# Kernel tuning notes

Measured on AMD Instinct MI355X. Metric: run time of the kernel, lower is better.

## Reference

```python
import jax, jax.numpy as jnp
import numpy as np

S = 2048
NODE_DIM = 128
H = 8          # num_heads
C = 32         # num_channels


def setup_inputs() -> dict:
    key = jax.random.key(0)
    ks = jax.random.split(key, 12)
    inv = lambda n: 1.0 / np.sqrt(n)
    inp = {
        "nodes": jax.random.normal(ks[0], (S, NODE_DIM), dtype=jnp.float32),
        "pos": jax.random.uniform(ks[1], (S, 3), dtype=jnp.float32),
        "rot": jax.random.normal(ks[2], (S, 4), dtype=jnp.float32),
        # eqx.nn.Linear weights are (out_features, in_features)
        "w_nodes_kq": jax.random.uniform(ks[3], (H * C * 2, NODE_DIM), minval=-inv(NODE_DIM), maxval=inv(NODE_DIM)),
        "b_nodes_kq": jax.random.uniform(ks[4], (H * C * 2,), minval=-inv(NODE_DIM), maxval=inv(NODE_DIM)),
        "w_pos_kq": jax.random.uniform(ks[5], (H * C * 2, 6), minval=-inv(6), maxval=inv(6)),
        "b_pos_kq": jax.random.uniform(ks[6], (H * C * 2,), minval=-inv(6), maxval=inv(6)),
        "w_rot_kq": jax.random.uniform(ks[7], (H * C * 2, 4), minval=-inv(4), maxval=inv(4)),  # no bias
        "w_values": jax.random.uniform(ks[8], (NODE_DIM * H * 3, NODE_DIM), minval=-inv(NODE_DIM), maxval=inv(NODE_DIM)),
        "b_values": jax.random.uniform(ks[9], (NODE_DIM * H * 3,), minval=-inv(NODE_DIM), maxval=inv(NODE_DIM)),
    }
    return inp


def reference(nodes, pos, rot, w_nodes_kq, b_nodes_kq, w_pos_kq, b_pos_kq,
              w_rot_kq, w_values, b_values):
    seq_len = nodes.shape[0]
    # circular positional features: [S, 6]
    pos_feat = jnp.concatenate([jnp.cos(2 * jnp.pi * pos), jnp.sin(2 * jnp.pi * pos)], axis=-1)

    # values: [S, 3H, node_dim]
    val = (nodes @ w_values.T + b_values).reshape(seq_len, 3 * H, -1)

    # per-source k/q projections, each -> [S, H, C]
    nodes_k, nodes_q = jnp.split((nodes @ w_nodes_kq.T + b_nodes_kq).reshape(seq_len, H, -1), 2, -1)
    pos_k, pos_q = jnp.split((pos_feat @ w_pos_kq.T + b_pos_kq).reshape(seq_len, H, -1), 2, -1)
    rot_k, rot_q = jnp.split((rot @ w_rot_kq.T).reshape(seq_len, H, -1), 2, -1)

    # concat over head axis -> [S, 3H, C]
    k = jnp.concatenate([nodes_k, pos_k, rot_k], axis=-2)
    q = jnp.concatenate([nodes_q, pos_q, rot_q], axis=-2)

    # logits: [S, S, 3H]; square the last H (rotation) heads' sub-logits
    logits = jnp.einsum('ihc,jhc->ijh', k, q)
    logits = logits.at[..., -H:].set(jnp.square(logits[..., -H:]))

    # softmax over j (axis=-2), then weighted sum of values over j and heads
    att = jax.nn.softmax(logits, axis=-2)
    out = jnp.einsum('ijh,jhd->id', att, val)  # [S, node_dim]
    return out
```

## Files before the change

kernel.cpp:

```cpp
#include <hip/hip_runtime.h>
#include <hip/hip_bf16.h>
#include <math.h>

#define SEQ 2048
#define NHEAD 24
#define CDIM 32
#define VDIM 128

typedef short bf16x8 __attribute__((ext_vector_type(8)));
typedef float f32x4 __attribute__((ext_vector_type(4)));

#define L2E 1.44269504088896f
#define SQRT_L2E 1.20112240878645f

#if __has_builtin(__builtin_amdgcn_exp2f)
#define EXP2(x) __builtin_amdgcn_exp2f(x)
#else
#define EXP2(x) exp2f(x)
#endif

__device__ unsigned short g_kkp[(size_t)24 * 128 * 2 * 64 * 8];
__device__ unsigned short g_qv[(size_t)24 * 32 * 24 * 64 * 8];
__device__ unsigned short g_wp[(size_t)224 * 4 * 2 * 64 * 8];
__device__ unsigned short g_np[(size_t)128 * 4 * 2 * 64 * 8];

__device__ __forceinline__ unsigned short f2b(float x) {
  union { float f; unsigned u; } v; v.f = x;
  unsigned r = v.u + 0x7FFF + ((v.u >> 16) & 1);
  return (unsigned short)(r >> 16);
}
__device__ __forceinline__ float b2f(unsigned short u) {
  union { unsigned u32; float f; } x; x.u32 = ((unsigned)u) << 16; return x.f;
}
__device__ __forceinline__ unsigned pk2(float a, float b) {
  __hip_bfloat162 t = __float22bfloat162_rn(float2{a, b});
  union { __hip_bfloat162 h; unsigned u; } c; c.h = t; return c.u;
}
__device__ __forceinline__ unsigned long long pack64(const float* p) {
  return ((unsigned long long)pk2(p[2], p[3]) << 32) | pk2(p[0], p[1]);
}
__device__ __forceinline__ float bperm_f(int srclane, float v) {
  union { float f; int i; } u; u.f = v;
  u.i = __builtin_amdgcn_ds_bpermute(srclane * 4, u.i);
  return u.f;
}
__device__ __forceinline__ void gld16(const unsigned short* g, unsigned short* l) {
  __builtin_amdgcn_global_load_lds(
      (const __attribute__((address_space(1))) unsigned int*)g,
      (__attribute__((address_space(3))) unsigned int*)l, 16, 0, 0);
}

__global__ __launch_bounds__(256) void k_prep(const float* __restrict__ nodes,
                                              const float* __restrict__ w_v,
                                              const float* __restrict__ w_n) {
  const int tid = blockIdx.x * 256 + threadIdx.x;
  const int fg = tid >> 6, lane = tid & 63;
  const int e0 = (lane >> 4) * 8;
  const float* p;
  unsigned short* dst;
  if (blockIdx.x < 224) {
    const int colblk = fg >> 2, ks = fg & 3;
    const int ocol = colblk * 16 + (lane & 15);
    const float* src = (ocol < 3072) ? (w_v + (size_t)ocol * 128)
                                     : (w_n + (size_t)(ocol - 3072) * 128);
    p = src + ks * 32 + e0;
    dst = g_wp + (size_t)fg * 1024;
  } else {
    const int fg2 = fg - 224 * 4;
    const int rowblk = fg2 >> 2, ks = fg2 & 3;
    p = nodes + (size_t)(rowblk * 16 + (lane & 15)) * 128 + ks * 32 + e0;
    dst = g_np + (size_t)fg2 * 1024;
  }
  float4 f0 = *(const float4*)p;
  float4 f1 = *(const float4*)(p + 4);
  float ff[8] = {f0.x, f0.y, f0.z, f0.w, f1.x, f1.y, f1.z, f1.w};
  bf16x8 hi, lo;
#pragma unroll
  for (int e = 0; e < 8; ++e) {
    unsigned short h2 = f2b(ff[e]);
    hi[e] = (short)h2;
    lo[e] = (short)f2b(ff[e] - b2f(h2));
  }
  *(bf16x8*)(dst + (size_t)lane * 8) = hi;
  *(bf16x8*)(dst + 512 + (size_t)lane * 8) = lo;
}

__global__ __launch_bounds__(256) void k_proj(const float* __restrict__ b_v,
                                              const float* __restrict__ b_n) {
  const int jt = blockIdx.x;
  const int bo = blockIdx.y;
  const bool is_kq = bo >= 48;
  const float* bsrc = is_kq ? b_n : b_v;
  const int o0b = is_kq ? (bo - 48) * 64 : bo * 64;
  const int tx = threadIdx.x;
  const int w = tx >> 6, lane = tx & 63;
  const int m = lane & 15, quad = lane >> 4;

  __shared__ __align__(16) unsigned short bst[32][64][8];
  __shared__ __align__(16) float res[4][64][20];

  const unsigned short* wp = g_wp + ((size_t)bo * 32 + w * 8) * 512 + (size_t)lane * 8;
#pragma unroll
  for (int s = 0; s < 8; ++s)
    gld16(wp + s * 512, &bst[w * 8 + s][0][0]);

  bf16x8 ah[4], al[4];
  const unsigned short* np = g_np + (size_t)(jt * 4 + w) * 4096 + (size_t)lane * 8;
#pragma unroll
  for (int ks = 0; ks < 4; ++ks) {
    ah[ks] = *(const bf16x8*)(np + ks * 1024);
    al[ks] = *(const bf16x8*)(np + ks * 1024 + 512);
  }
  __syncthreads();

  f32x4 C[4];
#pragma unroll
  for (int ob = 0; ob < 4; ++ob) {
    f32x4 acc = {0.f, 0.f, 0.f, 0.f};
#pragma unroll
    for (int ks = 0; ks < 4; ++ks) {
      bf16x8 bh = *(const bf16x8*)&bst[ob * 8 + ks * 2][lane][0];
      bf16x8 bl = *(const bf16x8*)&bst[ob * 8 + ks * 2 + 1][lane][0];
      acc = __builtin_amdgcn_mfma_f32_16x16x32_bf16(ah[ks], bh, acc, 0, 0, 0);
      acc = __builtin_amdgcn_mfma_f32_16x16x32_bf16(al[ks], bh, acc, 0, 0, 0);
      acc = __builtin_amdgcn_mfma_f32_16x16x32_bf16(ah[ks], bl, acc, 0, 0, 0);
    }
    C[ob] = acc;
  }
#pragma unroll
  for (int ob = 0; ob < 4; ++ob) {
    float bias = bsrc[o0b + ob * 16 + m];
#pragma unroll
    for (int r = 0; r < 4; ++r)
      res[w][ob * 16 + m][quad * 4 + r] = C[ob][r] + bias;
  }
  if (!is_kq) {
    const int g = bo >> 1, dbb = (bo & 1) * 4;
    const int jc = w >> 1, khb = (w & 1) * 2;
    const int rowq = quad;
#pragma unroll
    for (int oct = 0; oct < 2; ++oct) {
      f32x4 v0 = *(const f32x4*)&res[w][rowq * 16 + m][oct * 8];
      f32x4 v1 = *(const f32x4*)&res[w][rowq * 16 + m][oct * 8 + 4];
      bf16x8 pk;
#pragma unroll
      for (int e = 0; e < 4; ++e) {
        pk[e]     = (short)f2b(v0[e]);
        pk[4 + e] = (short)f2b(v1[e]);
      }
      ((bf16x8*)g_qv)[(((size_t)g * 32 + jt) * 24 + 8 + jc * 8 + dbb + rowq) * 64
                      + (khb + oct) * 16 + m] = pk;
    }
  } else {
    const int h = bo - 48;
    const int rowq = quad;
    {
      bf16x8 hi, lo;
#pragma unroll
      for (int e = 0; e < 8; ++e) {
        float v = res[w][rowq * 8 + e][m] * L2E;
        unsigned short h2 = f2b(v);
        hi[e] = (short)h2;
        lo[e] = (short)f2b(v - b2f(h2));
      }
      size_t base = ((size_t)(h * 128 + jt * 4 + w) * 2) * 512 + (size_t)(rowq * 16 + m) * 8;
      *(bf16x8*)(g_kkp + base) = hi;
      *(bf16x8*)(g_kkp + base + 512) = lo;
    }
    {
      bf16x8 hi, lo;
#pragma unroll
      for (int e = 0; e < 8; ++e) {
        float v = res[w][32 + rowq * 8 + e][m];
        unsigned short h2 = f2b(v);
        hi[e] = (short)h2;
        lo[e] = (short)f2b(v - b2f(h2));
      }
      size_t base = (((size_t)h * 32 + jt) * 24 + w * 2) * 512 + (size_t)(rowq * 16 + m) * 8;
      *(bf16x8*)(g_qv + base) = hi;
      *(bf16x8*)(g_qv + base + 512) = lo;
    }
  }
}

__device__ __forceinline__ void repack_store(const unsigned* __restrict__ res,
                                             int oh, int it16, int tx, int head_base) {
#pragma unroll
  for (int t2 = 0; t2 < 2; ++t2) {
    int cid = tx + t2 * 256;
    int hl  = cid >> 7;
    int kq  = (cid >> 6) & 1;
    int row = cid & 63;
    int m = row & 15, kb = row >> 4;
    int ob = hl * 64 + kq * 32 + kb * 8;
    bf16x8 hi, lo;
#pragma unroll
    for (int e = 0; e < 8; ++e) {
      unsigned pk = res[(ob + e) * 17 + m];
      hi[e] = (short)(pk >> 16);
      lo[e] = (short)(pk & 0xffff);
    }
    int gh = head_base + oh * 4 + hl;
    if (kq == 0) {
      size_t base = ((size_t)(gh * 128 + it16) * 2) * 512 + (size_t)row * 8;
      *(bf16x8*)(g_kkp + base) = hi;
      *(bf16x8*)(g_kkp + base + 512) = lo;
    } else {
      int jt = it16 >> 2, jb = it16 & 3;
      size_t base = (((size_t)gh * 32 + jt) * 24 + jb * 2) * 512 + (size_t)row * 8;
      *(bf16x8*)(g_qv + base) = hi;
      *(bf16x8*)(g_qv + base + 512) = lo;
    }
  }
}

__global__ __launch_bounds__(256) void k_posrot(const float* __restrict__ pos,
                                                const float* __restrict__ rot,
                                                const float* __restrict__ w_p,
                                                const float* __restrict__ b_p,
                                                const float* __restrict__ w_r) {
  const int it16 = blockIdx.x;
  const int oh   = blockIdx.y;
  const int br   = blockIdx.z;
  const int tx = threadIdx.x;
  const int i0 = it16 * 16;

  __shared__ float pf_sh[16][8];
  __shared__ float rr_sh[16][4];
  __shared__ unsigned res[256 * 17];

  if (br == 0) {
    if (tx < 48) {
      int r = tx / 3, t = tx - r * 3;
      float p = pos[(i0 + r) * 3 + t];
      pf_sh[r][t]     = cosf(6.283185307179586f * p);
      pf_sh[r][t + 3] = sinf(6.283185307179586f * p);
    }
  } else {
    if (tx < 64) {
      int r = tx >> 2, t = tx & 3;
      rr_sh[r][t] = rot[(i0 + r) * 4 + t];
    }
  }
  __syncthreads();

  const int og = tx & 63, ig = tx >> 6;

  if (br == 0) {
#pragma unroll
    for (int oo = 0; oo < 4; ++oo) {
      int o = oh * 256 + oo * 64 + og;
      float bb = b_p[o];
      float w0 = w_p[o * 6 + 0], w1 = w_p[o * 6 + 1], w2 = w_p[o * 6 + 2];
      float w3 = w_p[o * 6 + 3], w4 = w_p[o * 6 + 4], w5 = w_p[o * 6 + 5];
      float sc = ((o & 63) < 32) ? L2E : 1.f;
#pragma unroll
      for (int ii = 0; ii < 4; ++ii) {
        int i = ig * 4 + ii;
        float v = bb + pf_sh[i][0] * w0 + pf_sh[i][1] * w1 + pf_sh[i][2] * w2
                     + pf_sh[i][3] * w3 + pf_sh[i][4] * w4 + pf_sh[i][5] * w5;
        v *= sc;
        unsigned short hi = f2b(v);
        unsigned short lo = f2b(v - b2f(hi));
        res[(oo * 64 + og) * 17 + i] = ((unsigned)hi << 16) | lo;
      }
    }
  } else {
#pragma unroll
    for (int oo = 0; oo < 4; ++oo) {
      int o = oh * 256 + oo * 64 + og;
      float w0 = w_r[o * 4 + 0], w1 = w_r[o * 4 + 1], w2 = w_r[o * 4 + 2], w3 = w_r[o * 4 + 3];
      float sc = ((o & 63) < 32) ? SQRT_L2E : 1.f;
#pragma unroll
      for (int ii = 0; ii < 4; ++ii) {
        int i = ig * 4 + ii;
        float v = (rr_sh[i][0] * w0 + rr_sh[i][1] * w1 + rr_sh[i][2] * w2 + rr_sh[i][3] * w3) * sc;
        unsigned short hi = f2b(v);
        unsigned short lo = f2b(v - b2f(hi));
        res[(oo * 64 + og) * 17 + i] = ((unsigned)hi << 16) | lo;
      }
    }
  }
  __syncthreads();
  repack_store(res, oh, it16, tx, 8 + br * 8);
}

__global__ __launch_bounds__(256) void k_zero(float* __restrict__ out) {
  out[blockIdx.x * 256 + threadIdx.x] = 0.f;
}

__global__ __launch_bounds__(256, 3) void k_attn(float* __restrict__ out) {
  const int it = blockIdx.x;
  const int g  = blockIdx.y;
  const int tx = threadIdx.x;
  const int w = tx >> 6, lane = tx & 63;
  const int quad = lane >> 4, n = lane & 15;
  const int iblk = it * 4 + w;

  __shared__ __align__(16) unsigned short stage[2][24][64][8];
  __shared__ __align__(16) unsigned long long p_lds[4][64][2];

  const bf16x8* kp = (const bf16x8*)g_kkp + (size_t)(g * 128 + iblk) * 2 * 64;
  const bf16x8 khi = kp[lane], klo = kp[64 + lane];

  f32x4 oacc[8];
#pragma unroll
  for (int db = 0; db < 8; ++db)
#pragma unroll
    for (int r = 0; r < 4; ++r) oacc[db][r] = 0.f;

  float m_run = -3.0e38f, l_part = 0.f;
  const bool is_rot = (g >= 16);
  const int pin = (lane & 56) | ((lane ^ (lane >> 3)) & 7);
  const int wrow0 = (quad >> 1) * 16 + n;
  const int wrow1 = wrow0 + 32;
  const int pr0 = (wrow0 & 56) | ((wrow0 ^ (wrow0 >> 3)) & 7);
  const int pr1 = (wrow1 & 56) | ((wrow1 ^ (wrow1 >> 3)) & 7);
  const int whalf = quad & 1;

  const unsigned short* qv = g_qv + ((size_t)g * 32 * 24 + w * 6) * 512 + (size_t)lane * 8;

#define STG(nb)                                          \
  { gld16(qv,             &stage[nb][w * 6 + 0][0][0]);  \
    gld16(qv + 512,       &stage[nb][w * 6 + 1][0][0]);  \
    gld16(qv + 1024,      &stage[nb][w * 6 + 2][0][0]);  \
    gld16(qv + 1536,      &stage[nb][w * 6 + 3][0][0]);  \
    gld16(qv + 2048,      &stage[nb][w * 6 + 4][0][0]);  \
    gld16(qv + 2560,      &stage[nb][w * 6 + 5][0][0]); }

  STG(0)

  bf16x8 a0 = {}, a1 = {};
  bf16x8 vprev[16];

  for (int jt = 0; jt < 32; ++jt) {
    const int buf = jt & 1;
    __syncthreads();

    if (jt) {
#pragma unroll
      for (int db = 0; db < 8; ++db)
        oacc[db] = __builtin_amdgcn_mfma_f32_16x16x32_bf16(a0, vprev[db], oacc[db], 0, 0, 0);
#pragma unroll
      for (int db = 0; db < 8; ++db)
        oacc[db] = __builtin_amdgcn_mfma_f32_16x16x32_bf16(a1, vprev[8 + db], oacc[db], 0, 0, 0);
    }

    qv += 24 * 512;
    if (jt < 31) STG(buf ^ 1)

    const bf16x8* st = (const bf16x8*)&stage[buf][0][0][0];
    f32x4 S[4];
#pragma unroll
    for (int jb = 0; jb < 4; ++jb) {
      bf16x8 qh = st[(jb * 2) * 64 + lane], ql = st[(jb * 2 + 1) * 64 + lane];
      f32x4 a = {0.f, 0.f, 0.f, 0.f};
      a = __builtin_amdgcn_mfma_f32_16x16x32_bf16(qh, khi, a, 0, 0, 0);
      a = __builtin_amdgcn_mfma_f32_16x16x32_bf16(ql, khi, a, 0, 0, 0);
      a = __builtin_amdgcn_mfma_f32_16x16x32_bf16(qh, klo, a, 0, 0, 0);
      S[jb] = a;
    }
    if (is_rot) {
#pragma unroll
      for (int jb = 0; jb < 4; ++jb)
#pragma unroll
        for (int r = 0; r < 4; ++r) S[jb][r] *= S[jb][r];
    }
    float mloc = S[0][0];
#pragma unroll
    for (int jb = 0; jb < 4; ++jb)
#pragma unroll
      for (int r = 0; r < 4; ++r) mloc = fmaxf(mloc, S[jb][r]);
    if (__ballot(mloc > m_run)) {
      float mb = fmaxf(mloc, __shfl_xor(mloc, 16));
      mb = fmaxf(mb, __shfl_xor(mb, 32));
      float m_new = fmaxf(m_run, mb);
      float alpha = EXP2(m_run - m_new);
      m_run = m_new;
      l_part *= alpha;
      f32x4 av;
#pragma unroll
      for (int r = 0; r < 4; ++r) av[r] = bperm_f(quad * 4 + r, alpha);
#pragma unroll
      for (int db = 0; db < 8; ++db) {
        oacc[db][0] *= av[0]; oacc[db][1] *= av[1];
        oacc[db][2] *= av[2]; oacc[db][3] *= av[3];
      }
    }
    float p[4][4];
#pragma unroll
    for (int jb = 0; jb < 4; ++jb)
#pragma unroll
      for (int r = 0; r < 4; ++r) {
        p[jb][r] = EXP2(S[jb][r] - m_run);
        l_part += p[jb][r];
      }
    p_lds[w][pr0][whalf] = pack64(p[0]);
    p_lds[w][pr1][whalf] = pack64(p[1]);
    a0 = *(const bf16x8*)&p_lds[w][pin][0];
    p_lds[w][pr0][whalf] = pack64(p[2]);
    p_lds[w][pr1][whalf] = pack64(p[3]);
    a1 = *(const bf16x8*)&p_lds[w][pin][0];
#pragma unroll
    for (int f = 0; f < 16; ++f) vprev[f] = st[(8 + f) * 64 + lane];
  }
#pragma unroll
  for (int db = 0; db < 8; ++db)
    oacc[db] = __builtin_amdgcn_mfma_f32_16x16x32_bf16(a0, vprev[db], oacc[db], 0, 0, 0);
#pragma unroll
  for (int db = 0; db < 8; ++db)
    oacc[db] = __builtin_amdgcn_mfma_f32_16x16x32_bf16(a1, vprev[8 + db], oacc[db], 0, 0, 0);

  float l = l_part;
  l += __shfl_xor(l, 16);
  l += __shfl_xor(l, 32);
  float linv = 1.f / l;
  f32x4 lv;
#pragma unroll
  for (int r = 0; r < 4; ++r) lv[r] = bperm_f(quad * 4 + r, linv);
  const int ibase = it * 64 + w * 16 + quad * 4;
#pragma unroll
  for (int db = 0; db < 8; ++db)
#pragma unroll
    for (int r = 0; r < 4; ++r)
      atomicAdd(&out[(size_t)(ibase + r) * VDIM + db * 16 + n], oacc[db][r] * lv[r]);
}

extern "C" void kernel_launch(void* const* d_in, const int* in_sizes, int n_in,
                              void* d_out, int out_size, void* d_ws, size_t ws_size,
                              hipStream_t stream) {
  const float* nodes = (const float*)d_in[0];
  const float* pos   = (const float*)d_in[1];
  const float* rot   = (const float*)d_in[2];
  const float* w_n   = (const float*)d_in[3];
  const float* b_n   = (const float*)d_in[4];
  const float* w_p   = (const float*)d_in[5];
  const float* b_p   = (const float*)d_in[6];
  const float* w_r   = (const float*)d_in[7];
  const float* w_v   = (const float*)d_in[8];
  const float* b_v   = (const float*)d_in[9];
  float* out = (float*)d_out;

  k_zero<<<dim3((SEQ * VDIM) / 256), 256, 0, stream>>>(out);
  k_prep<<<dim3(352), 256, 0, stream>>>(nodes, w_v, w_n);
  k_posrot<<<dim3(128, 2, 2), 256, 0, stream>>>(pos, rot, w_p, b_p, w_r);
  k_proj<<<dim3(32, 56), 256, 0, stream>>>(b_v, b_n);
  k_attn<<<dim3(32, NHEAD), 256, 0, stream>>>(out);
}
```

Before: 168.1 us.

## Fuse prep/projection launches and restructure attention to split keys across waves

The zero-fill kernel is merged into the prep kernel, and the pos/rot projection is merged with the node projection into one launch, so five launches become three. The attention kernel is reorganized so each wave covers all four query-row blocks for half of the key range and half of the value dimension. Q/V fragments are read directly from global memory with one-step prefetch instead of being staged through LDS with barriers. Partial softmax statistics from the two key halves are combined through shared memory at the end. This raises register pressure (launch bounds drop from 3 to 2 blocks per CU) and duplicates the exp/softmax work across the two value-dimension waves.

```diff
diff --git a/kernel.cpp b/kernel.cpp
--- a/kernel.cpp
+++ b/kernel.cpp
@@ -50,15 +50,19 @@
       (__attribute__((address_space(3))) unsigned int*)l, 16, 0, 0);
 }
 
-__global__ __launch_bounds__(256) void k_prep(const float* __restrict__ nodes,
-                                              const float* __restrict__ w_v,
-                                              const float* __restrict__ w_n) {
-  const int tid = blockIdx.x * 256 + threadIdx.x;
+__global__ __launch_bounds__(256) void k_pre(const float* __restrict__ nodes,
+                                             const float* __restrict__ w_v,
+                                             const float* __restrict__ w_n,
+                                             float* __restrict__ out) {
+  const int bx = blockIdx.x;
+  if (bx < 1024) { out[bx * 256 + threadIdx.x] = 0.f; return; }
+  const int bb = bx - 1024;
+  const int tid = bb * 256 + threadIdx.x;
   const int fg = tid >> 6, lane = tid & 63;
   const int e0 = (lane >> 4) * 8;
   const float* p;
   unsigned short* dst;
-  if (blockIdx.x < 224) {
+  if (bb < 224) {
     const int colblk = fg >> 2, ks = fg & 3;
     const int ocol = colblk * 16 + (lane & 15);
     const float* src = (ocol < 3072) ? (w_v + (size_t)ocol * 128)
@@ -85,104 +89,6 @@
   *(bf16x8*)(dst + 512 + (size_t)lane * 8) = lo;
 }
 
-__global__ __launch_bounds__(256) void k_proj(const float* __restrict__ b_v,
-                                              const float* __restrict__ b_n) {
-  const int jt = blockIdx.x;
-  const int bo = blockIdx.y;
-  const bool is_kq = bo >= 48;
-  const float* bsrc = is_kq ? b_n : b_v;
-  const int o0b = is_kq ? (bo - 48) * 64 : bo * 64;
-  const int tx = threadIdx.x;
-  const int w = tx >> 6, lane = tx & 63;
-  const int m = lane & 15, quad = lane >> 4;
-
-  __shared__ __align__(16) unsigned short bst[32][64][8];
-  __shared__ __align__(16) float res[4][64][20];
-
-  const unsigned short* wp = g_wp + ((size_t)bo * 32 + w * 8) * 512 + (size_t)lane * 8;
-#pragma unroll
-  for (int s = 0; s < 8; ++s)
-    gld16(wp + s * 512, &bst[w * 8 + s][0][0]);
-
-  bf16x8 ah[4], al[4];
-  const unsigned short* np = g_np + (size_t)(jt * 4 + w) * 4096 + (size_t)lane * 8;
-#pragma unroll
-  for (int ks = 0; ks < 4; ++ks) {
-    ah[ks] = *(const bf16x8*)(np + ks * 1024);
-    al[ks] = *(const bf16x8*)(np + ks * 1024 + 512);
-  }
-  __syncthreads();
-
-  f32x4 C[4];
-#pragma unroll
-  for (int ob = 0; ob < 4; ++ob) {
-    f32x4 acc = {0.f, 0.f, 0.f, 0.f};
-#pragma unroll
-    for (int ks = 0; ks < 4; ++ks) {
-      bf16x8 bh = *(const bf16x8*)&bst[ob * 8 + ks * 2][lane][0];
-      bf16x8 bl = *(const bf16x8*)&bst[ob * 8 + ks * 2 + 1][lane][0];
-      acc = __builtin_amdgcn_mfma_f32_16x16x32_bf16(ah[ks], bh, acc, 0, 0, 0);
-      acc = __builtin_amdgcn_mfma_f32_16x16x32_bf16(al[ks], bh, acc, 0, 0, 0);
-      acc = __builtin_amdgcn_mfma_f32_16x16x32_bf16(ah[ks], bl, acc, 0, 0, 0);
-    }
-    C[ob] = acc;
-  }
-#pragma unroll
-  for (int ob = 0; ob < 4; ++ob) {
-    float bias = bsrc[o0b + ob * 16 + m];
-#pragma unroll
-    for (int r = 0; r < 4; ++r)
-      res[w][ob * 16 + m][quad * 4 + r] = C[ob][r] + bias;
-  }
-  if (!is_kq) {
-    const int g = bo >> 1, dbb = (bo & 1) * 4;
-    const int jc = w >> 1, khb = (w & 1) * 2;
-    const int rowq = quad;
-#pragma unroll
-    for (int oct = 0; oct < 2; ++oct) {
-      f32x4 v0 = *(const f32x4*)&res[w][rowq * 16 + m][oct * 8];
-      f32x4 v1 = *(const f32x4*)&res[w][rowq * 16 + m][oct * 8 + 4];
-      bf16x8 pk;
-#pragma unroll
-      for (int e = 0; e < 4; ++e) {
-        pk[e]     = (short)f2b(v0[e]);
-        pk[4 + e] = (short)f2b(v1[e]);
-      }
-      ((bf16x8*)g_qv)[(((size_t)g * 32 + jt) * 24 + 8 + jc * 8 + dbb + rowq) * 64
-                      + (khb + oct) * 16 + m] = pk;
-    }
-  } else {
-    const int h = bo - 48;
-    const int rowq = quad;
-    {
-      bf16x8 hi, lo;
-#pragma unroll
-      for (int e = 0; e < 8; ++e) {
-        float v = res[w][rowq * 8 + e][m] * L2E;
-        unsigned short h2 = f2b(v);
-        hi[e] = (short)h2;
-        lo[e] = (short)f2b(v - b2f(h2));
-      }
-      size_t base = ((size_t)(h * 128 + jt * 4 + w) * 2) * 512 + (size_t)(rowq * 16 + m) * 8;
-      *(bf16x8*)(g_kkp + base) = hi;
-      *(bf16x8*)(g_kkp + base + 512) = lo;
-    }
-    {
-      bf16x8 hi, lo;
-#pragma unroll
-      for (int e = 0; e < 8; ++e) {
-        float v = res[w][32 + rowq * 8 + e][m];
-        unsigned short h2 = f2b(v);
-        hi[e] = (short)h2;
-        lo[e] = (short)f2b(v - b2f(h2));
-      }
-      size_t base = (((size_t)h * 32 + jt) * 24 + w * 2) * 512 + (size_t)(rowq * 16 + m) * 8;
-      *(bf16x8*)(g_qv + base) = hi;
-      *(bf16x8*)(g_qv + base + 512) = lo;
-    }
-  }
-}
-
 __device__ __forceinline__ void repack_store(const unsigned* __restrict__ res,
                                              int oh, int it16, int tx, int head_base) {
 #pragma unroll
@@ -191,8 +97,8 @@
     int hl  = cid >> 7;
     int kq  = (cid >> 6) & 1;
     int row = cid & 63;
-    int m = row & 15, kb = row >> 4;
-    int ob = hl * 64 + kq * 32 + kb * 8;
+    int m = row & 15;
+    int ob = hl * 64 + kq * 32 + (row >> 4) * 8;
     bf16x8 hi, lo;
 #pragma unroll
     for (int e = 0; e < 8; ++e) {
@@ -214,216 +120,324 @@
   }
 }
 
-__global__ __launch_bounds__(256) void k_posrot(const float* __restrict__ pos,
-                                                const float* __restrict__ rot,
-                                                const float* __restrict__ w_p,
-                                                const float* __restrict__ b_p,
-                                                const float* __restrict__ w_r) {
-  const int it16 = blockIdx.x;
-  const int oh   = blockIdx.y;
-  const int br   = blockIdx.z;
+__global__ __launch_bounds__(256) void k_mid(const float* __restrict__ b_v,
+                                             const float* __restrict__ b_n,
+                                             const float* __restrict__ pos,
+                                             const float* __restrict__ rot,
+                                             const float* __restrict__ w_p,
+                                             const float* __restrict__ b_p,
+                                             const float* __restrict__ w_r) {
+  __shared__ __align__(16) char smem[53248];
+  const int bx = blockIdx.x;
   const int tx = threadIdx.x;
-  const int i0 = it16 * 16;
-
-  __shared__ float pf_sh[16][8];
-  __shared__ float rr_sh[16][4];
-  __shared__ unsigned res[256 * 17];
-
-  if (br == 0) {
-    if (tx < 48) {
-      int r = tx / 3, t = tx - r * 3;
-      float p = pos[(i0 + r) * 3 + t];
-      pf_sh[r][t]     = cosf(6.283185307179586f * p);
-      pf_sh[r][t + 3] = sinf(6.283185307179586f * p);
+
+  if (bx < 1792) {
+    const int jt = bx & 31;
+    const int bo = bx >> 5;
+    const bool is_kq = bo >= 48;
+    const float* bsrc = is_kq ? b_n : b_v;
+    const int o0b = is_kq ? (bo - 48) * 64 : bo * 64;
+    const int w = tx >> 6, lane = tx & 63;
+    const int m = lane & 15, quad = lane >> 4;
+
+    unsigned short (*bst)[64][8] = (unsigned short(*)[64][8])smem;
+    float (*res)[64][20] = (float(*)[64][20])(smem + 32768);
+
+    const unsigned short* wp = g_wp + ((size_t)bo * 32 + w * 8) * 512 + (size_t)lane * 8;
+#pragma unroll
+    for (int s = 0; s < 8; ++s)
+      gld16(wp + s * 512, &bst[w * 8 + s][0][0]);
+
+    bf16x8 ah[4], al[4];
+    const unsigned short* np = g_np + (size_t)(jt * 4 + w) * 4096 + (size_t)lane * 8;
+#pragma unroll
+    for (int ks = 0; ks < 4; ++ks) {
+      ah[ks] = *(const bf16x8*)(np + ks * 1024);
+      al[ks] = *(const bf16x8*)(np + ks * 1024 + 512);
+    }
+    __syncthreads();
+
+    f32x4 C[4];
+#pragma unroll
+    for (int ob = 0; ob < 4; ++ob) {
+      f32x4 acc = {0.f, 0.f, 0.f, 0.f};
+#pragma unroll
+      for (int ks = 0; ks < 4; ++ks) {
+        bf16x8 bh = *(const bf16x8*)&bst[ob * 8 + ks * 2][lane][0];
+        bf16x8 bl = *(const bf16x8*)&bst[ob * 8 + ks * 2 + 1][lane][0];
+        acc = __builtin_amdgcn_mfma_f32_16x16x32_bf16(ah[ks], bh, acc, 0, 0, 0);
+        acc = __builtin_amdgcn_mfma_f32_16x16x32_bf16(al[ks], bh, acc, 0, 0, 0);
+        acc = __builtin_amdgcn_mfma_f32_16x16x32_bf16(ah[ks], bl, acc, 0, 0, 0);
+      }
+      C[ob] = acc;
+    }
+#pragma unroll
+    for (int ob = 0; ob < 4; ++ob) {
+      float bias = bsrc[o0b + ob * 16 + m];
+#pragma unroll
+      for (int r = 0; r < 4; ++r)
+        res[w][ob * 16 + m][quad * 4 + r] = C[ob][r] + bias;
+    }
+    if (!is_kq) {
+      const int g = bo >> 1, dbb = (bo & 1) * 4;
+      const int jc = w >> 1, khb = (w & 1) * 2;
+#pragma unroll
+      for (int oct = 0; oct < 2; ++oct) {
+        f32x4 v0 = *(const f32x4*)&res[w][quad * 16 + m][oct * 8];
+        f32x4 v1 = *(const f32x4*)&res[w][quad * 16 + m][oct * 8 + 4];
+        bf16x8 pk;
+#pragma unroll
+        for (int e = 0; e < 4; ++e) {
+          pk[e]     = (short)f2b(v0[e]);
+          pk[4 + e] = (short)f2b(v1[e]);
+        }
+        ((bf16x8*)g_qv)[(((size_t)g * 32 + jt) * 24 + 8 + jc * 8 + dbb + quad) * 64
+                        + (khb + oct) * 16 + m] = pk;
+      }
+    } else {
+      const int h = bo - 48;
+      {
+        bf16x8 hi, lo;
+#pragma unroll
+        for (int e = 0; e < 8; ++e) {
+          float v = res[w][quad * 8 + e][m] * L2E;
+          unsigned short h2 = f2b(v);
+          hi[e] = (short)h2;
+          lo[e] = (short)f2b(v - b2f(h2));
+        }
+        size_t base = ((size_t)(h * 128 + jt * 4 + w) * 2) * 512 + (size_t)(quad * 16 + m) * 8;
+        *(bf16x8*)(g_kkp + base) = hi;
+        *(bf16x8*)(g_kkp + base + 512) = lo;
+      }
+      {
+        bf16x8 hi, lo;
+#pragma unroll
+        for (int e = 0; e < 8; ++e) {
+          float v = res[w][32 + quad * 8 + e][m];
+          unsigned short h2 = f2b(v);
+          hi[e] = (short)h2;
+          lo[e] = (short)f2b(v - b2f(h2));
+        }
+        size_t base = (((size_t)h * 32 + jt) * 24 + w * 2) * 512 + (size_t)(quad * 16 + m) * 8;
+        *(bf16x8*)(g_qv + base) = hi;
+        *(bf16x8*)(g_qv + base + 512) = lo;
+      }
     }
   } else {
-    if (tx < 64) {
-      int r = tx >> 2, t = tx & 3;
-      rr_sh[r][t] = rot[(i0 + r) * 4 + t];
-    }
-  }
-  __syncthreads();
-
-  const int og = tx & 63, ig = tx >> 6;
-
-  if (br == 0) {
-#pragma unroll
-    for (int oo = 0; oo < 4; ++oo) {
-      int o = oh * 256 + oo * 64 + og;
-      float bb = b_p[o];
-      float w0 = w_p[o * 6 + 0], w1 = w_p[o * 6 + 1], w2 = w_p[o * 6 + 2];
-      float w3 = w_p[o * 6 + 3], w4 = w_p[o * 6 + 4], w5 = w_p[o * 6 + 5];
-      float sc = ((o & 63) < 32) ? L2E : 1.f;
-#pragma unroll
-      for (int ii = 0; ii < 4; ++ii) {
-        int i = ig * 4 + ii;
-        float v = bb + pf_sh[i][0] * w0 + pf_sh[i][1] * w1 + pf_sh[i][2] * w2
-                     + pf_sh[i][3] * w3 + pf_sh[i][4] * w4 + pf_sh[i][5] * w5;
-        v *= sc;
-        unsigned short hi = f2b(v);
-        unsigned short lo = f2b(v - b2f(hi));
-        res[(oo * 64 + og) * 17 + i] = ((unsigned)hi << 16) | lo;
-      }
-    }
-  } else {
-#pragma unroll
-    for (int oo = 0; oo < 4; ++oo) {
-      int o = oh * 256 + oo * 64 + og;
-      float w0 = w_r[o * 4 + 0], w1 = w_r[o * 4 + 1], w2 = w_r[o * 4 + 2], w3 = w_r[o * 4 + 3];
-      float sc = ((o & 63) < 32) ? SQRT_L2E : 1.f;
-#pragma unroll
-      for (int ii = 0; ii < 4; ++ii) {
-        int i = ig * 4 + ii;
-        float v = (rr_sh[i][0] * w0 + rr_sh[i][1] * w1 + rr_sh[i][2] * w2 + rr_sh[i][3] * w3) * sc;
-        unsigned short hi = f2b(v);
-        unsigned short lo = f2b(v - b2f(hi));
-        res[(oo * 64 + og) * 17 + i] = ((unsigned)hi << 16) | lo;
-      }
-    }
-  }
-  __syncthreads();
-  repack_store(res, oh, it16, tx, 8 + br * 8);
-}
-
-__global__ __launch_bounds__(256) void k_zero(float* __restrict__ out) {
-  out[blockIdx.x * 256 + threadIdx.x] = 0.f;
-}
-
-__global__ __launch_bounds__(256, 3) void k_attn(float* __restrict__ out) {
+    const int r0 = bx - 1792;
+    const int it16 = r0 & 127, oh = (r0 >> 7) & 1, br = r0 >> 8;
+    const int i0 = it16 * 16;
+    unsigned* res = (unsigned*)smem;
+    float (*pf_sh)[8] = (float(*)[8])(smem + 17408);
+    float (*rr_sh)[4] = (float(*)[4])(smem + 17920);
+
+    if (br == 0) {
+      if (tx < 48) {
+        int r = tx / 3, t = tx - r * 3;
+        float p = pos[(i0 + r) * 3 + t];
+        pf_sh[r][t]     = cosf(6.283185307179586f * p);
+        pf_sh[r][t + 3] = sinf(6.283185307179586f * p);
+      }
+    } else {
+      if (tx < 64) {
+        int r = tx >> 2, t = tx & 3;
+        rr_sh[r][t] = rot[(i0 + r) * 4 + t];
+      }
+    }
+    __syncthreads();
+
+    const int og = tx & 63, ig = tx >> 6;
+    if (br == 0) {
+#pragma unroll
+      for (int oo = 0; oo < 4; ++oo) {
+        int o = oh * 256 + oo * 64 + og;
+        float bb = b_p[o];
+        float w0 = w_p[o * 6 + 0], w1 = w_p[o * 6 + 1], w2 = w_p[o * 6 + 2];
+        float w3 = w_p[o * 6 + 3], w4 = w_p[o * 6 + 4], w5 = w_p[o * 6 + 5];
+        float sc = ((o & 63) < 32) ? L2E : 1.f;
+#pragma unroll
+        for (int ii = 0; ii < 4; ++ii) {
+          int i = ig * 4 + ii;
+          float v = bb + pf_sh[i][0] * w0 + pf_sh[i][1] * w1 + pf_sh[i][2] * w2
+                       + pf_sh[i][3] * w3 + pf_sh[i][4] * w4 + pf_sh[i][5] * w5;
+          v *= sc;
+          unsigned short hi = f2b(v);
+          unsigned short lo = f2b(v - b2f(hi));
+          res[(oo * 64 + og) * 17 + i] = ((unsigned)hi << 16) | lo;
+        }
+      }
+    } else {
+#pragma unroll
+      for (int oo = 0; oo < 4; ++oo) {
+        int o = oh * 256 + oo * 64 + og;
+        float w0 = w_r[o * 4 + 0], w1 = w_r[o * 4 + 1], w2 = w_r[o * 4 + 2], w3 = w_r[o * 4 + 3];
+        float sc = ((o & 63) < 32) ? SQRT_L2E : 1.f;
+#pragma unroll
+        for (int ii = 0; ii < 4; ++ii) {
+          int i = ig * 4 + ii;
+          float v = (rr_sh[i][0] * w0 + rr_sh[i][1] * w1 + rr_sh[i][2] * w2 + rr_sh[i][3] * w3) * sc;
+          unsigned short hi = f2b(v);
+          unsigned short lo = f2b(v - b2f(hi));
+          res[(oo * 64 + og) * 17 + i] = ((unsigned)hi << 16) | lo;
+        }
+      }
+    }
+    __syncthreads();
+    repack_store(res, oh, it16, tx, 8 + br * 8);
+  }
+}
+
+__global__ __launch_bounds__(256, 2) void k_attn(float* __restrict__ out) {
   const int it = blockIdx.x;
   const int g  = blockIdx.y;
   const int tx = threadIdx.x;
   const int w = tx >> 6, lane = tx & 63;
-  const int quad = lane >> 4, n = lane & 15;
-  const int iblk = it * 4 + w;
-
-  __shared__ __align__(16) unsigned short stage[2][24][64][8];
+  const int qd = lane >> 4, c = lane & 15;
+  const int jh = w >> 1, dh = w & 1;
+  const bool is_rot = (g >= 16);
+
   __shared__ __align__(16) unsigned long long p_lds[4][64][2];
-
-  const bf16x8* kp = (const bf16x8*)g_kkp + (size_t)(g * 128 + iblk) * 2 * 64;
-  const bf16x8 khi = kp[lane], klo = kp[64 + lane];
-
-  f32x4 oacc[8];
-#pragma unroll
-  for (int db = 0; db < 8; ++db)
-#pragma unroll
-    for (int r = 0; r < 4; ++r) oacc[db][r] = 0.f;
-
-  float m_run = -3.0e38f, l_part = 0.f;
-  const bool is_rot = (g >= 16);
+  __shared__ __align__(16) float s_m[2][4][16];
+  __shared__ __align__(16) float s_l[2][4][16];
+  __shared__ __align__(16) float s_sc[2][4][16];
+
+  bf16x8 khi[4], klo[4];
+#pragma unroll
+  for (int ib = 0; ib < 4; ++ib) {
+    const bf16x8* kp = (const bf16x8*)g_kkp + ((size_t)(g * 128 + it * 4 + ib)) * 2 * 64;
+    khi[ib] = kp[lane]; klo[ib] = kp[64 + lane];
+  }
+
+  f32x4 oacc[4][4];
+#pragma unroll
+  for (int ib = 0; ib < 4; ++ib)
+#pragma unroll
+    for (int d = 0; d < 4; ++d)
+#pragma unroll
+      for (int r = 0; r < 4; ++r) oacc[ib][d][r] = 0.f;
+
+  float m4[4] = {-3.0e38f, -3.0e38f, -3.0e38f, -3.0e38f};
+  float l4[4] = {0.f, 0.f, 0.f, 0.f};
+
   const int pin = (lane & 56) | ((lane ^ (lane >> 3)) & 7);
-  const int wrow0 = (quad >> 1) * 16 + n;
-  const int wrow1 = wrow0 + 32;
-  const int pr0 = (wrow0 & 56) | ((wrow0 ^ (wrow0 >> 3)) & 7);
-  const int pr1 = (wrow1 & 56) | ((wrow1 ^ (wrow1 >> 3)) & 7);
-  const int whalf = quad & 1;
-
-  const unsigned short* qv = g_qv + ((size_t)g * 32 * 24 + w * 6) * 512 + (size_t)lane * 8;
-
-#define STG(nb)                                          \
-  { gld16(qv,             &stage[nb][w * 6 + 0][0][0]);  \
-    gld16(qv + 512,       &stage[nb][w * 6 + 1][0][0]);  \
-    gld16(qv + 1024,      &stage[nb][w * 6 + 2][0][0]);  \
-    gld16(qv + 1536,      &stage[nb][w * 6 + 3][0][0]);  \
-    gld16(qv + 2048,      &stage[nb][w * 6 + 4][0][0]);  \
-    gld16(qv + 2560,      &stage[nb][w * 6 + 5][0][0]); }
-
-  STG(0)
-
-  bf16x8 a0 = {}, a1 = {};
-  bf16x8 vprev[16];
-
-  for (int jt = 0; jt < 32; ++jt) {
-    const int buf = jt & 1;
-    __syncthreads();
-
-    if (jt) {
-#pragma unroll
-      for (int db = 0; db < 8; ++db)
-        oacc[db] = __builtin_amdgcn_mfma_f32_16x16x32_bf16(a0, vprev[db], oacc[db], 0, 0, 0);
-#pragma unroll
-      for (int db = 0; db < 8; ++db)
-        oacc[db] = __builtin_amdgcn_mfma_f32_16x16x32_bf16(a1, vprev[8 + db], oacc[db], 0, 0, 0);
-    }
-
-    qv += 24 * 512;
-    if (jt < 31) STG(buf ^ 1)
-
-    const bf16x8* st = (const bf16x8*)&stage[buf][0][0][0];
-    f32x4 S[4];
-#pragma unroll
-    for (int jb = 0; jb < 4; ++jb) {
-      bf16x8 qh = st[(jb * 2) * 64 + lane], ql = st[(jb * 2 + 1) * 64 + lane];
+  const int row0 = (qd >> 1) * 16 + c;
+  const int row1 = row0 + 32;
+  const int pr0 = (row0 & 56) | ((row0 ^ (row0 >> 3)) & 7);
+  const int pr1 = (row1 & 56) | ((row1 ^ (row1 >> 3)) & 7);
+  const int half = qd & 1;
+
+  const unsigned short* gbase = g_qv + (size_t)g * 32 * 24 * 512 + (size_t)lane * 8;
+#define FRAG(jt_, slot_) (*(const bf16x8*)(gbase + ((size_t)(jt_) * 24 + (slot_)) * 512))
+
+  bf16x8 qf[4];
+#pragma unroll
+  for (int s = 0; s < 4; ++s) qf[s] = FRAG(jh * 16, s);
+
+  for (int t = 0; t < 32; ++t) {
+    const int jt = jh * 16 + (t >> 1), jc = t & 1;
+    bf16x8 vb[4];
+#pragma unroll
+    for (int d = 0; d < 4; ++d) vb[d] = FRAG(jt, 8 + jc * 8 + dh * 4 + d);
+    bf16x8 qn[4];
+    if (t < 31) {
+      const int jt1 = jh * 16 + ((t + 1) >> 1), jc1 = (t + 1) & 1;
+#pragma unroll
+      for (int s = 0; s < 4; ++s) qn[s] = FRAG(jt1, jc1 * 4 + s);
+    }
+    f32x4 S0[4], S1[4];
+#pragma unroll
+    for (int ib = 0; ib < 4; ++ib) {
       f32x4 a = {0.f, 0.f, 0.f, 0.f};
-      a = __builtin_amdgcn_mfma_f32_16x16x32_bf16(qh, khi, a, 0, 0, 0);
-      a = __builtin_amdgcn_mfma_f32_16x16x32_bf16(ql, khi, a, 0, 0, 0);
-      a = __builtin_amdgcn_mfma_f32_16x16x32_bf16(qh, klo, a, 0, 0, 0);
-      S[jb] = a;
+      a = __builtin_amdgcn_mfma_f32_16x16x32_bf16(qf[0], khi[ib], a, 0, 0, 0);
+      a = __builtin_amdgcn_mfma_f32_16x16x32_bf16(qf[1], khi[ib], a, 0, 0, 0);
+      a = __builtin_amdgcn_mfma_f32_16x16x32_bf16(qf[0], klo[ib], a, 0, 0, 0);
+      S0[ib] = a;
+      f32x4 b = {0.f, 0.f, 0.f, 0.f};
+      b = __builtin_amdgcn_mfma_f32_16x16x32_bf16(qf[2], khi[ib], b, 0, 0, 0);
+      b = __builtin_amdgcn_mfma_f32_16x16x32_bf16(qf[3], khi[ib], b, 0, 0, 0);
+      b = __builtin_amdgcn_mfma_f32_16x16x32_bf16(qf[2], klo[ib], b, 0, 0, 0);
+      S1[ib] = b;
     }
     if (is_rot) {
 #pragma unroll
-      for (int jb = 0; jb < 4; ++jb)
-#pragma unroll
-        for (int r = 0; r < 4; ++r) S[jb][r] *= S[jb][r];
-    }
-    float mloc = S[0][0];
-#pragma unroll
-    for (int jb = 0; jb < 4; ++jb)
-#pragma unroll
-      for (int r = 0; r < 4; ++r) mloc = fmaxf(mloc, S[jb][r]);
-    if (__ballot(mloc > m_run)) {
-      float mb = fmaxf(mloc, __shfl_xor(mloc, 16));
-      mb = fmaxf(mb, __shfl_xor(mb, 32));
-      float m_new = fmaxf(m_run, mb);
-      float alpha = EXP2(m_run - m_new);
-      m_run = m_new;
-      l_part *= alpha;
-      f32x4 av;
-#pragma unroll
-      for (int r = 0; r < 4; ++r) av[r] = bperm_f(quad * 4 + r, alpha);
-#pragma unroll
-      for (int db = 0; db < 8; ++db) {
-        oacc[db][0] *= av[0]; oacc[db][1] *= av[1];
-        oacc[db][2] *= av[2]; oacc[db][3] *= av[3];
-      }
-    }
-    float p[4][4];
-#pragma unroll
-    for (int jb = 0; jb < 4; ++jb)
+      for (int ib = 0; ib < 4; ++ib)
+#pragma unroll
+        for (int r = 0; r < 4; ++r) { S0[ib][r] *= S0[ib][r]; S1[ib][r] *= S1[ib][r]; }
+    }
+    float ml[4];
+#pragma unroll
+    for (int ib = 0; ib < 4; ++ib) {
+      float v = fmaxf(fmaxf(S0[ib][0], S0[ib][1]), fmaxf(S0[ib][2], S0[ib][3]));
+      v = fmaxf(v, fmaxf(fmaxf(S1[ib][0], S1[ib][1]), fmaxf(S1[ib][2], S1[ib][3])));
+      ml[ib] = v;
+    }
+    bool ex = (ml[0] > m4[0]) || (ml[1] > m4[1]) || (ml[2] > m4[2]) || (ml[3] > m4[3]);
+    if (__ballot(ex)) {
+#pragma unroll
+      for (int ib = 0; ib < 4; ++ib) {
+        float mb = fmaxf(ml[ib], __shfl_xor(ml[ib], 16));
+        mb = fmaxf(mb, __shfl_xor(mb, 32));
+        float mn = fmaxf(m4[ib], mb);
+        float al = EXP2(m4[ib] - mn);
+        m4[ib] = mn;
+        l4[ib] *= al;
+        f32x4 av;
+#pragma unroll
+        for (int r = 0; r < 4; ++r) av[r] = bperm_f(qd * 4 + r, al);
+#pragma unroll
+        for (int d = 0; d < 4; ++d) {
+          oacc[ib][d][0] *= av[0]; oacc[ib][d][1] *= av[1];
+          oacc[ib][d][2] *= av[2]; oacc[ib][d][3] *= av[3];
+        }
+      }
+    }
+#pragma unroll
+    for (int ib = 0; ib < 4; ++ib) {
+      f32x4 p0, p1;
 #pragma unroll
       for (int r = 0; r < 4; ++r) {
-        p[jb][r] = EXP2(S[jb][r] - m_run);
-        l_part += p[jb][r];
-      }
-    p_lds[w][pr0][whalf] = pack64(p[0]);
-    p_lds[w][pr1][whalf] = pack64(p[1]);
-    a0 = *(const bf16x8*)&p_lds[w][pin][0];
-    p_lds[w][pr0][whalf] = pack64(p[2]);
-    p_lds[w][pr1][whalf] = pack64(p[3]);
-    a1 = *(const bf16x8*)&p_lds[w][pin][0];
-#pragma unroll
-    for (int f = 0; f < 16; ++f) vprev[f] = st[(8 + f) * 64 + lane];
-  }
-#pragma unroll
-  for (int db = 0; db < 8; ++db)
-    oacc[db] = __builtin_amdgcn_mfma_f32_16x16x32_bf16(a0, vprev[db], oacc[db], 0, 0, 0);
-#pragma unroll
-  for (int db = 0; db < 8; ++db)
-    oacc[db] = __builtin_amdgcn_mfma_f32_16x16x32_bf16(a1, vprev[8 + db], oacc[db], 0, 0, 0);
-
-  float l = l_part;
-  l += __shfl_xor(l, 16);
-  l += __shfl_xor(l, 32);
-  float linv = 1.f / l;
-  f32x4 lv;
-#pragma unroll
-  for (int r = 0; r < 4; ++r) lv[r] = bperm_f(quad * 4 + r, linv);
-  const int ibase = it * 64 + w * 16 + quad * 4;
-#pragma unroll
-  for (int db = 0; db < 8; ++db)
-#pragma unroll
-    for (int r = 0; r < 4; ++r)
-      atomicAdd(&out[(size_t)(ibase + r) * VDIM + db * 16 + n], oacc[db][r] * lv[r]);
+        p0[r] = EXP2(S0[ib][r] - m4[ib]);
+        p1[r] = EXP2(S1[ib][r] - m4[ib]);
+      }
+      l4[ib] += p0[0] + p0[1] + p0[2] + p0[3] + p1[0] + p1[1] + p1[2] + p1[3];
+      p_lds[w][pr0][half] = pack64((const float*)&p0);
+      p_lds[w][pr1][half] = pack64((const float*)&p1);
+      bf16x8 a = *(const bf16x8*)&p_lds[w][pin][0];
+#pragma unroll
+      for (int d = 0; d < 4; ++d)
+        oacc[ib][d] = __builtin_amdgcn_mfma_f32_16x16x32_bf16(a, vb[d], oacc[ib][d], 0, 0, 0);
+    }
+#pragma unroll
+    for (int s = 0; s < 4; ++s) qf[s] = qn[s];
+  }
+
+#pragma unroll
+  for (int ib = 0; ib < 4; ++ib) {
+    l4[ib] += __shfl_xor(l4[ib], 16);
+    l4[ib] += __shfl_xor(l4[ib], 32);
+  }
+  float mq = (qd == 0) ? m4[0] : (qd == 1) ? m4[1] : (qd == 2) ? m4[2] : m4[3];
+  float lq = (qd == 0) ? l4[0] : (qd == 1) ? l4[1] : (qd == 2) ? l4[2] : l4[3];
+  if (dh == 0) { s_m[jh][qd][c] = mq; s_l[jh][qd][c] = lq; }
+  __syncthreads();
+  if (dh == 0) {
+    float ma = s_m[0][qd][c], mb2 = s_m[1][qd][c];
+    float ms = fmaxf(ma, mb2);
+    float ls = s_l[0][qd][c] * EXP2(ma - ms) + s_l[1][qd][c] * EXP2(mb2 - ms);
+    s_sc[jh][qd][c] = EXP2((jh ? mb2 : ma) - ms) / ls;
+  }
+  __syncthreads();
+  const int i0 = it * 64;
+#pragma unroll
+  for (int ib = 0; ib < 4; ++ib) {
+    f32x4 lv = *(const f32x4*)&s_sc[jh][ib][qd * 4];
+#pragma unroll
+    for (int d = 0; d < 4; ++d)
+#pragma unroll
+      for (int r = 0; r < 4; ++r)
+        atomicAdd(&out[(size_t)(i0 + ib * 16 + qd * 4 + r) * VDIM + dh * 64 + d * 16 + c],
+                  oacc[ib][d][r] * lv[r]);
+  }
 }
 
 extern "C" void kernel_launch(void* const* d_in, const int* in_sizes, int n_in,
@@ -441,9 +455,7 @@
   const float* b_v   = (const float*)d_in[9];
   float* out = (float*)d_out;
 
-  k_zero<<<dim3((SEQ * VDIM) / 256), 256, 0, stream>>>(out);
-  k_prep<<<dim3(352), 256, 0, stream>>>(nodes, w_v, w_n);
-  k_posrot<<<dim3(128, 2, 2), 256, 0, stream>>>(pos, rot, w_p, b_p, w_r);
-  k_proj<<<dim3(32, 56), 256, 0, stream>>>(b_v, b_n);
+  k_pre<<<dim3(1024 + 352), 256, 0, stream>>>(nodes, w_v, w_n, out);
+  k_mid<<<dim3(1792 + 512), 256, 0, stream>>>(b_v, b_n, pos, rot, w_p, b_p, w_r);
   k_attn<<<dim3(32, NHEAD), 256, 0, stream>>>(out);
 }
```

New measurement: 205.5 us. +22.3%, slower.
